# Kernel optimization log

Hardware: AMD Instinct MI355X
Metric: run time of the kernel (lower is better)

The kernel has to match this reference:

```python
import jax, jax.numpy as jnp
import numpy as np

N_PAPER, N_MESH = 60000, 30000
N = N_PAPER + N_MESH
E_TRAIN, E_DEC = 2000000, 400000
F_PAPER = F_MESH = 128
D0, H, D = 16, 32, 16  # initial embed, hidden, final embed
NREL, NB = 2, 4


def _glorot(key, shape):
    fan_in, fan_out = shape[-2], shape[-1]
    s = jnp.sqrt(6.0 / (fan_in + fan_out)).astype(jnp.float32)
    return jax.random.uniform(key, shape, jnp.float32, -s, s)


def setup_inputs() -> dict:
    key = jax.random.key(0)
    ks = iter(jax.random.split(key, 40))
    inp = {
        'x_paper': jax.random.normal(next(ks), (N_PAPER, F_PAPER), jnp.float32),
        'x_mesh': jax.random.normal(next(ks), (N_MESH, F_MESH), jnp.float32),
        'train_edge_index': jax.random.randint(next(ks), (2, E_TRAIN), 0, N, jnp.int64 if jax.config.jax_enable_x64 else jnp.int32),
        'train_edge_type': jnp.sort(jax.random.randint(next(ks), (E_TRAIN,), 0, NREL)),
        'pos_edge_index': jax.random.randint(next(ks), (2, E_DEC), 0, N),
        'pos_edge_type': jnp.sort(jax.random.randint(next(ks), (E_DEC,), 0, NREL)),
        'neg_edge_index': jax.random.randint(next(ks), (2, E_DEC), 0, N),
        'neg_edge_type': jnp.sort(jax.random.randint(next(ks), (E_DEC,), 0, NREL)),
        # input transforms
        'Wp': _glorot(next(ks), (F_PAPER, D0)), 'bp': jnp.zeros((D0,), jnp.float32),
        'Wm': _glorot(next(ks), (F_MESH, D0)), 'bm': jnp.zeros((D0,), jnp.float32),
        # decode linears
        'Wd0': _glorot(next(ks), (D, D)), 'bd0': jnp.zeros((D,), jnp.float32),
        'Wd1': _glorot(next(ks), (D, D)), 'bd1': jnp.zeros((D,), jnp.float32),
    }
    dims = [(D0, H), (H, H), (H, H), (H, D)]
    for i, (di, do) in enumerate(dims, 1):
        inp[f'bases{i}'] = _glorot(next(ks), (NB, di, do))
        inp[f'comp{i}'] = _glorot(next(ks), (NREL, NB))
        inp[f'root{i}'] = _glorot(next(ks), (di, do))
        inp[f'bias{i}'] = jnp.zeros((do,), jnp.float32)
    return inp


def rgcn_layer(x, src, dst, et, bases, comp, root, bias):
    # PyG RGCNConv with basis decomposition, per-relation mean aggregation.
    out = x @ root + bias
    xs = x[src]  # [E, in]
    for r in range(NREL):
        W_r = jnp.einsum('b,bio->io', comp[r], bases)
        m = xs @ W_r  # [E, out]
        mf = (et == r).astype(m.dtype)
        cnt = jax.ops.segment_sum(mf, dst, num_segments=N)
        agg = jax.ops.segment_sum(m * mf[:, None], dst, num_segments=N)
        out = out + agg / jnp.clip(cnt, 1.0)[:, None]
    return out


def _decode_block(z, ei, et, Wd0, bd0, Wd1, bd1):
    zs, zd = z[ei[0]], z[ei[1]]
    h0 = zs @ Wd0 + bd0
    h1 = zs @ Wd1 + bd1
    h = jnp.where((et == 0)[:, None], h0, h1)
    return jnp.sum(h * zd, axis=-1)


def reference(x_paper, x_mesh, train_edge_index, train_edge_type,
              pos_edge_index, pos_edge_type, neg_edge_index, neg_edge_type,
              Wp, bp, Wm, bm, Wd0, bd0, Wd1, bd1,
              bases1, comp1, root1, bias1, bases2, comp2, root2, bias2,
              bases3, comp3, root3, bias3, bases4, comp4, root4, bias4):
    x = jnp.concatenate([x_paper @ Wp + bp, x_mesh @ Wm + bm], axis=0)  # [N, D0]
    src, dst = train_edge_index[0], train_edge_index[1]
    x = jax.nn.relu(rgcn_layer(x, src, dst, train_edge_type, bases1, comp1, root1, bias1))
    x = jax.nn.relu(rgcn_layer(x, src, dst, train_edge_type, bases2, comp2, root2, bias2))
    x = jax.nn.relu(rgcn_layer(x, src, dst, train_edge_type, bases3, comp3, root3, bias3))
    z = rgcn_layer(x, src, dst, train_edge_type, bases4, comp4, root4, bias4)
    # edge types are sorted, so per-edge in-order compute matches the masked concat order
    pos = _decode_block(z, pos_edge_index, pos_edge_type, Wd0, bd0, Wd1, bd1)
    neg = _decode_block(z, neg_edge_index, neg_edge_type, Wd0, bd0, Wd1, bd1)
    return jnp.concatenate([pos, neg], axis=0)  # [2*E_DEC]
```

## Files before the change

kernel.cpp:

```cpp
#include <hip/hip_runtime.h>
#include <hip/hip_bf16.h>

constexpr int NN = 90000;
constexpr int NP = 60000;
constexpr int NM = 30000;
constexpr int ET = 2000000;
constexpr int ED = 400000;
constexpr int TWO_NN = 2 * NN;

constexpr int BKT_SH  = 10;
constexpr int NB_BKT  = (TWO_NN + 1023) >> BKT_SH;
constexpr int BKT_CAP = 12288;
constexpr int TILE    = 2048;
constexpr int N_TILES = (ET + TILE - 1) / TILE;

__device__ __forceinline__ float bf2f(unsigned short u) {
    union { unsigned int i; float f; } c;
    c.i = ((unsigned int)u) << 16;
    return c.f;
}
__device__ __forceinline__ unsigned short f2bf(float f) {
    union { float f; unsigned int i; } c;
    c.f = f;
    unsigned int x = c.i;
    return (unsigned short)((x + 0x7FFFu + ((x >> 16) & 1u)) >> 16);
}

__global__ void detect_kernel(const int* __restrict__ tei, int* __restrict__ flag) {
    if (blockIdx.x == 0 && threadIdx.x == 0) {
        int allzero = 1;
        for (int i = 0; i < 16; i++)
            if (tei[2 * i + 1] != 0) allzero = 0;
        flag[0] = allzero;
    }
}

__global__ void init_gcur_kernel(int* __restrict__ gcur) {
    int b = blockIdx.x * blockDim.x + threadIdx.x;
    if (b < NB_BKT) gcur[b] = b * BKT_CAP;
}

__global__ void __launch_bounds__(256) binA_kernel(
        const int* __restrict__ ei, const int* __restrict__ et,
        const int* __restrict__ dflag, int* __restrict__ gcur,
        int2* __restrict__ pairs) {
    __shared__ int hist[NB_BKT];
    __shared__ int excl[NB_BKT];
    __shared__ int cur[NB_BKT];
    __shared__ int gbase[NB_BKT];
    __shared__ int scn[256];
    __shared__ int2 tbuf[TILE];
    int t = threadIdx.x;
    int tile0 = blockIdx.x * TILE;
    int tcount = ET - tile0;
    if (tcount > TILE) tcount = TILE;
    for (int i = t; i < NB_BKT; i += 256) hist[i] = 0;
    __syncthreads();
    int sft = dflag[0];
    int myk[8], mys[8];
#pragma unroll
    for (int q = 0; q < 8; q++) {
        int li = q * 256 + t;
        myk[q] = -1;
        if (li < tcount) {
            int e = tile0 + li;
            int s = ei[(size_t)e << sft];
            int d = ei[(size_t)(ET + e) << sft];
            int r = et[(size_t)e << sft];
            int key = r * NN + d;
            myk[q] = key;
            mys[q] = s;
            atomicAdd(&hist[key >> BKT_SH], 1);
        }
    }
    __syncthreads();
    int v = (t < NB_BKT) ? hist[t] : 0;
    scn[t] = v;
    __syncthreads();
    for (int st = 1; st < 256; st <<= 1) {
        int u = (t >= st) ? scn[t - st] : 0;
        __syncthreads();
        scn[t] += u;
        __syncthreads();
    }
    if (t < NB_BKT) {
        excl[t] = scn[t] - v;
        cur[t] = scn[t] - v;
    }
    __syncthreads();
#pragma unroll
    for (int q = 0; q < 8; q++) {
        if (myk[q] >= 0) {
            int b = myk[q] >> BKT_SH;
            int p = atomicAdd(&cur[b], 1);
            tbuf[p] = make_int2(myk[q], mys[q]);
        }
    }
    __syncthreads();
    if (t < NB_BKT && hist[t] > 0) gbase[t] = atomicAdd(&gcur[t], hist[t]);
    __syncthreads();
    for (int i = t; i < tcount; i += 256) {
        int2 p = tbuf[i];
        int b = p.x >> BKT_SH;
        int gpos = gbase[b] + (i - excl[b]);
        int cap = (b + 1) * BKT_CAP - 1;
        pairs[gpos < cap ? gpos : cap] = p;
    }
}

__global__ void __launch_bounds__(256) histB_kernel(
        const int* __restrict__ gcur, const int2* __restrict__ pairs,
        int* __restrict__ off, int* __restrict__ endo, float* __restrict__ inv) {
    __shared__ int kh[1024];
    __shared__ int scn[256];
    int b = blockIdx.x;
    int t = threadIdx.x;
    for (int i = t; i < 1024; i += 256) kh[i] = 0;
    __syncthreads();
    int beg = b * BKT_CAP, end = gcur[b];
    for (int i = beg + t; i < end; i += 256)
        atomicAdd(&kh[pairs[i].x & 1023], 1);
    __syncthreads();
    int v[4];
    int s = 0;
#pragma unroll
    for (int q = 0; q < 4; q++) {
        v[q] = kh[t * 4 + q];
        s += v[q];
    }
    scn[t] = s;
    __syncthreads();
    for (int st = 1; st < 256; st <<= 1) {
        int u = (t >= st) ? scn[t - st] : 0;
        __syncthreads();
        scn[t] += u;
        __syncthreads();
    }
    int run = b * BKT_CAP + scn[t] - s;
    int kbase = b << BKT_SH;
#pragma unroll
    for (int q = 0; q < 4; q++) {
        int key = kbase + t * 4 + q;
        if (key < TWO_NN) {
            off[key] = run;
            endo[key] = run + v[q];
            inv[key] = 1.0f / (float)(v[q] > 1 ? v[q] : 1);
        }
        run += v[q];
    }
}

__global__ void __launch_bounds__(256) placeB_kernel(
        const int* __restrict__ gcur, const int2* __restrict__ pairs,
        const int* __restrict__ off, int* __restrict__ csr) {
    __shared__ int kc[1024];
    int b = blockIdx.x;
    int t = threadIdx.x;
    int kbase = b << BKT_SH;
    for (int i = t; i < 1024; i += 256)
        if (kbase + i < TWO_NN) kc[i] = off[kbase + i];
    __syncthreads();
    int beg = b * BKT_CAP, end = gcur[b];
    for (int i = beg + t; i < end; i += 256) {
        int2 p = pairs[i];
        int pos = atomicAdd(&kc[p.x & 1023], 1);
        csr[pos] = p.y;
    }
}

__global__ void __launch_bounds__(256) embed2_kernel(
        const float* __restrict__ Xp, const float* __restrict__ Xm,
        const float* __restrict__ Wp, const float* __restrict__ bp,
        const float* __restrict__ Wm, const float* __restrict__ bm,
        float* __restrict__ out, unsigned short* __restrict__ outbf) {
    __shared__ float Wl[4096 + 32];
    for (int i = threadIdx.x; i < 2048; i += 256) {
        Wl[i] = Wp[i];
        Wl[2048 + i] = Wm[i];
    }
    if (threadIdx.x < 16) {
        Wl[4096 + threadIdx.x] = bp[threadIdx.x];
        Wl[4112 + threadIdx.x] = bm[threadIdx.x];
    }
    __syncthreads();
    int n = blockIdx.x * 256 + threadIdx.x;
    if (n >= NN) return;
    const float* X;
    const float* Ws;
    const float* Bs;
    if (n < NP) { X = Xp + (size_t)n * 128; Ws = Wl; Bs = Wl + 4096; }
    else        { X = Xm + (size_t)(n - NP) * 128; Ws = Wl + 2048; Bs = Wl + 4112; }
    float acc[16];
#pragma unroll
    for (int j = 0; j < 16; j++) acc[j] = Bs[j];
    const float4* row = (const float4*)X;
    for (int k4 = 0; k4 < 32; k4++) {
        float4 xv = row[k4];
        int k = k4 * 4;
#pragma unroll
        for (int j = 0; j < 16; j++) {
            float a = acc[j];
            a = fmaf(xv.x, Ws[(k + 0) * 16 + j], a);
            a = fmaf(xv.y, Ws[(k + 1) * 16 + j], a);
            a = fmaf(xv.z, Ws[(k + 2) * 16 + j], a);
            a = fmaf(xv.w, Ws[(k + 3) * 16 + j], a);
            acc[j] = a;
        }
    }
    float4* o = (float4*)(out + (size_t)n * 16);
    ushort4* ob = (ushort4*)(outbf + (size_t)n * 16);
#pragma unroll
    for (int q = 0; q < 4; q++) {
        o[q] = make_float4(acc[4 * q], acc[4 * q + 1], acc[4 * q + 2], acc[4 * q + 3]);
        ushort4 ub;
        ub.x = f2bf(acc[4 * q]);     ub.y = f2bf(acc[4 * q + 1]);
        ub.z = f2bf(acc[4 * q + 2]); ub.w = f2bf(acc[4 * q + 3]);
        ob[q] = ub;
    }
}

__global__ void prep_all_kernel(
        const float* __restrict__ ba0, const float* __restrict__ co0,
        const float* __restrict__ ro0, const float* __restrict__ bi0,
        const float* __restrict__ ba1, const float* __restrict__ co1,
        const float* __restrict__ ro1, const float* __restrict__ bi1,
        const float* __restrict__ ba2, const float* __restrict__ co2,
        const float* __restrict__ ro2, const float* __restrict__ bi2,
        const float* __restrict__ ba3, const float* __restrict__ co3,
        const float* __restrict__ ro3, const float* __restrict__ bi3,
        float* __restrict__ Wbuf4) {
    int l = blockIdx.x;
    const float* bases; const float* comp; const float* root; const float* bias;
    if (l == 0)      { bases = ba0; comp = co0; root = ro0; bias = bi0; }
    else if (l == 1) { bases = ba1; comp = co1; root = ro1; bias = bi1; }
    else if (l == 2) { bases = ba2; comp = co2; root = ro2; bias = bi2; }
    else             { bases = ba3; comp = co3; root = ro3; bias = bi3; }
    int din = (l == 0) ? 16 : 32;
    int dout = (l == 3) ? 16 : 32;
    int sz = din * dout;
    float* W = Wbuf4 + l * 3200;
    for (int i = threadIdx.x; i < sz; i += 256) {
        float b0 = bases[i];
        float b1 = bases[sz + i];
        float b2 = bases[2 * sz + i];
        float b3 = bases[3 * sz + i];
        for (int r = 0; r < 2; r++) {
            W[r * sz + i] = comp[r * 4 + 0] * b0 + comp[r * 4 + 1] * b1 +
                            comp[r * 4 + 2] * b2 + comp[r * 4 + 3] * b3;
        }
        W[2 * sz + i] = root[i];
    }
    if (threadIdx.x < dout) W[3 * sz + threadIdx.x] = bias[threadIdx.x];
}

template <int DIN, int DOUT, int RELU, int WBF>
__global__ void __launch_bounds__(256) layer_kernel(
        const int* __restrict__ off, const int* __restrict__ endo,
        const int* __restrict__ csr,
        const float* __restrict__ xin, const unsigned short* __restrict__ xbf_in,
        const float* __restrict__ inv, const float* __restrict__ Wbuf,
        float* __restrict__ xout, unsigned short* __restrict__ xbf_out) {
    constexpr int SZ = DIN * DOUT;
    constexpr int QL = DIN / 4;
    constexpr int TPN = 2 * QL;
    constexpr int NPB = 256 / TPN;
    constexpr int AGST = 2 * DIN + 4;
    constexpr int XSST = DIN + 4;
    __shared__ float Wl[3 * SZ + DOUT];
    __shared__ float agg[NPB * AGST];
    __shared__ float xs[NPB * XSST];
    for (int i = threadIdx.x; i < 3 * SZ + DOUT; i += 256) Wl[i] = Wbuf[i];
    int t = threadIdx.x;
    int ln = t / TPN;
    int rl = t % TPN;
    int r = rl / QL;
    int lane = rl % QL;
    int d = blockIdx.x * NPB + ln;
    if (d < NN) {
        if (r == 0)
            *(float4*)(xs + ln * XSST + lane * 4) =
                *(const float4*)(xin + (size_t)d * DIN + lane * 4);
        int key = r * NN + d;
        int b = off[key];
        int e = endo[key];
        float4 a0 = make_float4(0, 0, 0, 0), a1 = make_float4(0, 0, 0, 0);
        float4 a2 = make_float4(0, 0, 0, 0), a3 = make_float4(0, 0, 0, 0);
        const unsigned short* hp = xbf_in + lane * 4;
        int k = b;
        for (; k + 3 < e; k += 4) {
            int s0 = csr[k];
            int s1 = csr[k + 1];
            int s2 = csr[k + 2];
            int s3 = csr[k + 3];
            ushort4 u0 = *(const ushort4*)(hp + (size_t)s0 * DIN);
            ushort4 u1 = *(const ushort4*)(hp + (size_t)s1 * DIN);
            ushort4 u2 = *(const ushort4*)(hp + (size_t)s2 * DIN);
            ushort4 u3 = *(const ushort4*)(hp + (size_t)s3 * DIN);
            a0.x += bf2f(u0.x); a0.y += bf2f(u0.y); a0.z += bf2f(u0.z); a0.w += bf2f(u0.w);
            a1.x += bf2f(u1.x); a1.y += bf2f(u1.y); a1.z += bf2f(u1.z); a1.w += bf2f(u1.w);
            a2.x += bf2f(u2.x); a2.y += bf2f(u2.y); a2.z += bf2f(u2.z); a2.w += bf2f(u2.w);
            a3.x += bf2f(u3.x); a3.y += bf2f(u3.y); a3.z += bf2f(u3.z); a3.w += bf2f(u3.w);
        }
        for (; k < e; k++) {
            ushort4 u0 = *(const ushort4*)(hp + (size_t)csr[k] * DIN);
            a0.x += bf2f(u0.x); a0.y += bf2f(u0.y); a0.z += bf2f(u0.z); a0.w += bf2f(u0.w);
        }
        *(float4*)(agg + ln * AGST + r * DIN + lane * 4) =
            make_float4(a0.x + a1.x + a2.x + a3.x, a0.y + a1.y + a2.y + a3.y,
                        a0.z + a1.z + a2.z + a3.z, a0.w + a1.w + a2.w + a3.w);
    }
    __syncthreads();
    constexpr int CPN = DOUT / 4;
    if (t < NPB * CPN) {
        int ln2 = t / CPN;
        int j0 = (t % CPN) * 4;
        int d2 = blockIdx.x * NPB + ln2;
        if (d2 < NN) {
            float iv0 = inv[d2], iv1 = inv[NN + d2];
            float acc[4];
#pragma unroll
            for (int jj = 0; jj < 4; jj++) acc[jj] = Wl[3 * SZ + j0 + jj];
#pragma unroll
            for (int k = 0; k < DIN; k++) {
                float xv = xs[ln2 * XSST + k];
                float a0 = agg[ln2 * AGST + k] * iv0;
                float a1 = agg[ln2 * AGST + DIN + k] * iv1;
                const float* w0 = &Wl[k * DOUT + j0];
                const float* w1 = &Wl[SZ + k * DOUT + j0];
                const float* wr = &Wl[2 * SZ + k * DOUT + j0];
#pragma unroll
                for (int jj = 0; jj < 4; jj++) {
                    acc[jj] = fmaf(xv, wr[jj], acc[jj]);
                    acc[jj] = fmaf(a0, w0[jj], acc[jj]);
                    acc[jj] = fmaf(a1, w1[jj], acc[jj]);
                }
            }
            if (RELU) {
#pragma unroll
                for (int jj = 0; jj < 4; jj++) acc[jj] = fmaxf(acc[jj], 0.0f);
            }
            *(float4*)(xout + (size_t)d2 * DOUT + j0) =
                make_float4(acc[0], acc[1], acc[2], acc[3]);
            if (WBF) {
                ushort4 ub;
                ub.x = f2bf(acc[0]); ub.y = f2bf(acc[1]);
                ub.z = f2bf(acc[2]); ub.w = f2bf(acc[3]);
                *(ushort4*)(xbf_out + (size_t)d2 * DOUT + j0) = ub;
            }
        }
    }
}

__global__ void decode_prep_kernel(const float* __restrict__ z,
                                   const float* __restrict__ Wd0,
                                   const float* __restrict__ bd0,
                                   const float* __restrict__ Wd1,
                                   const float* __restrict__ bd1,
                                   float* __restrict__ y0, float* __restrict__ y1) {
    __shared__ float W0l[256], W1l[256], B0[16], B1[16];
    for (int i = threadIdx.x; i < 256; i += blockDim.x) {
        W0l[i] = Wd0[i];
        W1l[i] = Wd1[i];
    }
    if (threadIdx.x < 16) {
        B0[threadIdx.x] = bd0[threadIdx.x];
        B1[threadIdx.x] = bd1[threadIdx.x];
    }
    __syncthreads();
    int n = blockIdx.x * blockDim.x + threadIdx.x;
    if (n >= NN) return;
    float zr[16];
    const float* zp = z + (size_t)n * 16;
#pragma unroll
    for (int k = 0; k < 16; k++) zr[k] = zp[k];
    float o0[16], o1[16];
#pragma unroll
    for (int j = 0; j < 16; j++) {
        float a0 = B0[j], a1 = B1[j];
#pragma unroll
        for (int k = 0; k < 16; k++) {
            a0 = fmaf(zr[k], W0l[k * 16 + j], a0);
            a1 = fmaf(zr[k], W1l[k * 16 + j], a1);
        }
        o0[j] = a0;
        o1[j] = a1;
    }
    float4* p0 = (float4*)(y0 + (size_t)n * 16);
    float4* p1 = (float4*)(y1 + (size_t)n * 16);
#pragma unroll
    for (int q = 0; q < 4; q++) {
        p0[q] = make_float4(o0[4 * q], o0[4 * q + 1], o0[4 * q + 2], o0[4 * q + 3]);
        p1[q] = make_float4(o1[4 * q], o1[4 * q + 1], o1[4 * q + 2], o1[4 * q + 3]);
    }
}

__global__ void decode_kernel(const float* __restrict__ y0, const float* __restrict__ y1,
                              const float* __restrict__ z,
                              const int* __restrict__ pei, const int* __restrict__ pet,
                              const int* __restrict__ nei, const int* __restrict__ net_,
                              float* __restrict__ out,
                              const int* __restrict__ dflag) {
    int i = blockIdx.x * blockDim.x + threadIdx.x;
    if (i >= 2 * ED) return;
    int sft = dflag[0];
    const int* ei;
    const int* et;
    int e;
    if (i < ED) { ei = pei; et = pet; e = i; }
    else        { ei = nei; et = net_; e = i - ED; }
    int s = ei[(size_t)e << sft];
    int d = ei[(size_t)(ED + e) << sft];
    int r = et[(size_t)e << sft];
    const float4* yv = (const float4*)((r ? y1 : y0) + ((size_t)s << 4));
    const float4* zv = (const float4*)(z + ((size_t)d << 4));
    float acc = 0.0f;
#pragma unroll
    for (int q = 0; q < 4; q++) {
        float4 a = yv[q];
        float4 b = zv[q];
        acc += a.x * b.x + a.y * b.y + a.z * b.z + a.w * b.w;
    }
    out[i] = acc;
}

extern "C" void kernel_launch(void* const* d_in, const int* in_sizes, int n_in,
                              void* d_out, int out_size, void* d_ws, size_t ws_size,
                              hipStream_t stream) {
    const float* x_paper = (const float*)d_in[0];
    const float* x_mesh  = (const float*)d_in[1];
    const int* tei  = (const int*)d_in[2];
    const int* tet  = (const int*)d_in[3];
    const int* pei  = (const int*)d_in[4];
    const int* pet  = (const int*)d_in[5];
    const int* nei  = (const int*)d_in[6];
    const int* net_ = (const int*)d_in[7];
    const float* Wp  = (const float*)d_in[8];
    const float* bp  = (const float*)d_in[9];
    const float* Wm  = (const float*)d_in[10];
    const float* bm  = (const float*)d_in[11];
    const float* Wd0 = (const float*)d_in[12];
    const float* bd0 = (const float*)d_in[13];
    const float* Wd1 = (const float*)d_in[14];
    const float* bd1 = (const float*)d_in[15];

    float* ws = (float*)d_ws;
    size_t o = 0;
    float* bufA = ws + o; o += (size_t)NN * 32;
    float* bufB = ws + o; o += (size_t)NN * 32;
    unsigned short* xbfA = (unsigned short*)(ws + o); o += (size_t)NN * 16;
    unsigned short* xbfB = (unsigned short*)(ws + o); o += (size_t)NN * 16;
    float* inv  = ws + o; o += (size_t)TWO_NN;
    int*   off  = (int*)(ws + o); o += (size_t)TWO_NN;
    int*   endo = (int*)(ws + o); o += (size_t)TWO_NN;
    int*   csr  = (int*)(ws + o); o += (size_t)NB_BKT * BKT_CAP;
    int*   gcur = (int*)(ws + o); o += 256;
    int2*  pairs = (int2*)(ws + o); o += (size_t)2 * NB_BKT * BKT_CAP;
    float* Wbuf4 = ws + o; o += 4 * 3200;
    int*   dflag = (int*)(ws + o); o += 16;

    detect_kernel<<<1, 64, 0, stream>>>(tei, dflag);

    init_gcur_kernel<<<1, 256, 0, stream>>>(gcur);
    binA_kernel<<<N_TILES, 256, 0, stream>>>(tei, tet, dflag, gcur, pairs);
    histB_kernel<<<NB_BKT, 256, 0, stream>>>(gcur, pairs, off, endo, inv);
    placeB_kernel<<<NB_BKT, 256, 0, stream>>>(gcur, pairs, off, csr);

    embed2_kernel<<<(NN + 255) / 256, 256, 0, stream>>>(
        x_paper, x_mesh, Wp, bp, Wm, bm, bufA, xbfA);

    prep_all_kernel<<<4, 256, 0, stream>>>(
        (const float*)d_in[16], (const float*)d_in[17], (const float*)d_in[18], (const float*)d_in[19],
        (const float*)d_in[20], (const float*)d_in[21], (const float*)d_in[22], (const float*)d_in[23],
        (const float*)d_in[24], (const float*)d_in[25], (const float*)d_in[26], (const float*)d_in[27],
        (const float*)d_in[28], (const float*)d_in[29], (const float*)d_in[30], (const float*)d_in[31],
        Wbuf4);

    int blk16 = (NN + 31) / 32;
    int blk32 = (NN + 15) / 16;
    layer_kernel<16, 32, 1, 1><<<blk16, 256, 0, stream>>>(
        off, endo, csr, bufA, xbfA, inv, Wbuf4 + 0 * 3200, bufB, xbfB);
    layer_kernel<32, 32, 1, 1><<<blk32, 256, 0, stream>>>(
        off, endo, csr, bufB, xbfB, inv, Wbuf4 + 1 * 3200, bufA, xbfA);
    layer_kernel<32, 32, 1, 1><<<blk32, 256, 0, stream>>>(
        off, endo, csr, bufA, xbfA, inv, Wbuf4 + 2 * 3200, bufB, xbfB);
    layer_kernel<32, 16, 0, 0><<<blk32, 256, 0, stream>>>(
        off, endo, csr, bufB, xbfB, inv, Wbuf4 + 3 * 3200, bufA, xbfA );

    float* y0 = bufB;
    float* y1 = bufB + (size_t)NN * 16;
    decode_prep_kernel<<<(NN + 255) / 256, 256, 0, stream>>>(bufA, Wd0, bd0, Wd1, bd1,
                                                             y0, y1);
    decode_kernel<<<(2 * ED + 255) / 256, 256, 0, stream>>>(
        y0, y1, bufA, pei, pet, nei, net_, (float*)d_out, dflag);
}
```

Measured before the change: 430.5 us.

## Widen gather loads to 16 bytes, fuse decode kernels, merge init kernels

The layer gather now has each thread load 8 bf16 values with one uint4 load instead of 4, so twice as many nodes fit in a block and the grid sizes halve. The decode prep and decode kernels are merged: each edge recomputes the 16x16 relation transform of the source embedding in registers instead of reading a precomputed y buffer. The detect and gcur-init kernels become one kernel. The changes cut launches and intermediate memory traffic, but add redundant per-edge FLOPs in decode and reduce memory-level parallelism per thread in the gather.

New measurement: 400.4 us. -7.0%, faster.

```diff
diff --git a/kernel.cpp b/kernel.cpp
--- a/kernel.cpp
+++ b/kernel.cpp
@@ -14,9 +14,14 @@
 constexpr int TILE    = 2048;
 constexpr int N_TILES = (ET + TILE - 1) / TILE;
 
-__device__ __forceinline__ float bf2f(unsigned short u) {
+__device__ __forceinline__ float bflo(unsigned int u) {
     union { unsigned int i; float f; } c;
-    c.i = ((unsigned int)u) << 16;
+    c.i = u << 16;
+    return c.f;
+}
+__device__ __forceinline__ float bfhi(unsigned int u) {
+    union { unsigned int i; float f; } c;
+    c.i = u & 0xffff0000u;
     return c.f;
 }
 __device__ __forceinline__ unsigned short f2bf(float f) {
@@ -26,18 +31,16 @@
     return (unsigned short)((x + 0x7FFFu + ((x >> 16) & 1u)) >> 16);
 }
 
-__global__ void detect_kernel(const int* __restrict__ tei, int* __restrict__ flag) {
-    if (blockIdx.x == 0 && threadIdx.x == 0) {
+__global__ void init_kernel(const int* __restrict__ tei, int* __restrict__ gcur,
+                            int* __restrict__ dflag) {
+    int b = blockIdx.x * blockDim.x + threadIdx.x;
+    if (b < NB_BKT) gcur[b] = b * BKT_CAP;
+    if (b == 0) {
         int allzero = 1;
         for (int i = 0; i < 16; i++)
             if (tei[2 * i + 1] != 0) allzero = 0;
-        flag[0] = allzero;
-    }
-}
-
-__global__ void init_gcur_kernel(int* __restrict__ gcur) {
-    int b = blockIdx.x * blockDim.x + threadIdx.x;
-    if (b < NB_BKT) gcur[b] = b * BKT_CAP;
+        dflag[0] = allzero;
+    }
 }
 
 __global__ void __launch_bounds__(256) binA_kernel(
@@ -261,7 +264,7 @@
         const float* __restrict__ inv, const float* __restrict__ Wbuf,
         float* __restrict__ xout, unsigned short* __restrict__ xbf_out) {
     constexpr int SZ = DIN * DOUT;
-    constexpr int QL = DIN / 4;
+    constexpr int QL = DIN / 8;
     constexpr int TPN = 2 * QL;
     constexpr int NPB = 256 / TPN;
     constexpr int AGST = 2 * DIN + 4;
@@ -277,43 +280,47 @@
     int lane = rl % QL;
     int d = blockIdx.x * NPB + ln;
     if (d < NN) {
-        if (r == 0)
-            *(float4*)(xs + ln * XSST + lane * 4) =
-                *(const float4*)(xin + (size_t)d * DIN + lane * 4);
+        *(float4*)(xs + ln * XSST + rl * 4) =
+            *(const float4*)(xin + (size_t)d * DIN + rl * 4);
         int key = r * NN + d;
         int b = off[key];
         int e = endo[key];
-        float4 a0 = make_float4(0, 0, 0, 0), a1 = make_float4(0, 0, 0, 0);
-        float4 a2 = make_float4(0, 0, 0, 0), a3 = make_float4(0, 0, 0, 0);
-        const unsigned short* hp = xbf_in + lane * 4;
+        float a0[8] = {0, 0, 0, 0, 0, 0, 0, 0};
+        float a1[8] = {0, 0, 0, 0, 0, 0, 0, 0};
+        const unsigned short* hp = xbf_in + lane * 8;
         int k = b;
-        for (; k + 3 < e; k += 4) {
+        for (; k + 1 < e; k += 2) {
             int s0 = csr[k];
             int s1 = csr[k + 1];
-            int s2 = csr[k + 2];
-            int s3 = csr[k + 3];
-            ushort4 u0 = *(const ushort4*)(hp + (size_t)s0 * DIN);
-            ushort4 u1 = *(const ushort4*)(hp + (size_t)s1 * DIN);
-            ushort4 u2 = *(const ushort4*)(hp + (size_t)s2 * DIN);
-            ushort4 u3 = *(const ushort4*)(hp + (size_t)s3 * DIN);
-            a0.x += bf2f(u0.x); a0.y += bf2f(u0.y); a0.z += bf2f(u0.z); a0.w += bf2f(u0.w);
-            a1.x += bf2f(u1.x); a1.y += bf2f(u1.y); a1.z += bf2f(u1.z); a1.w += bf2f(u1.w);
-            a2.x += bf2f(u2.x); a2.y += bf2f(u2.y); a2.z += bf2f(u2.z); a2.w += bf2f(u2.w);
-            a3.x += bf2f(u3.x); a3.y += bf2f(u3.y); a3.z += bf2f(u3.z); a3.w += bf2f(u3.w);
-        }
-        for (; k < e; k++) {
-            ushort4 u0 = *(const ushort4*)(hp + (size_t)csr[k] * DIN);
-            a0.x += bf2f(u0.x); a0.y += bf2f(u0.y); a0.z += bf2f(u0.z); a0.w += bf2f(u0.w);
-        }
-        *(float4*)(agg + ln * AGST + r * DIN + lane * 4) =
-            make_float4(a0.x + a1.x + a2.x + a3.x, a0.y + a1.y + a2.y + a3.y,
-                        a0.z + a1.z + a2.z + a3.z, a0.w + a1.w + a2.w + a3.w);
+            uint4 u0 = *(const uint4*)(hp + (size_t)s0 * DIN);
+            uint4 u1 = *(const uint4*)(hp + (size_t)s1 * DIN);
+            a0[0] += bflo(u0.x); a0[1] += bfhi(u0.x);
+            a0[2] += bflo(u0.y); a0[3] += bfhi(u0.y);
+            a0[4] += bflo(u0.z); a0[5] += bfhi(u0.z);
+            a0[6] += bflo(u0.w); a0[7] += bfhi(u0.w);
+            a1[0] += bflo(u1.x); a1[1] += bfhi(u1.x);
+            a1[2] += bflo(u1.y); a1[3] += bfhi(u1.y);
+            a1[4] += bflo(u1.z); a1[5] += bfhi(u1.z);
+            a1[6] += bflo(u1.w); a1[7] += bfhi(u1.w);
+        }
+        if (k < e) {
+            uint4 u0 = *(const uint4*)(hp + (size_t)csr[k] * DIN);
+            a0[0] += bflo(u0.x); a0[1] += bfhi(u0.x);
+            a0[2] += bflo(u0.y); a0[3] += bfhi(u0.y);
+            a0[4] += bflo(u0.z); a0[5] += bfhi(u0.z);
+            a0[6] += bflo(u0.w); a0[7] += bfhi(u0.w);
+        }
+        float* ap = agg + ln * AGST + r * DIN + lane * 8;
+        *(float4*)ap = make_float4(a0[0] + a1[0], a0[1] + a1[1],
+                                   a0[2] + a1[2], a0[3] + a1[3]);
+        *(float4*)(ap + 4) = make_float4(a0[4] + a1[4], a0[5] + a1[5],
+                                         a0[6] + a1[6], a0[7] + a1[7]);
     }
     __syncthreads();
     constexpr int CPN = DOUT / 4;
-    if (t < NPB * CPN) {
-        int ln2 = t / CPN;
-        int j0 = (t % CPN) * 4;
+    for (int tt = t; tt < NPB * CPN; tt += 256) {
+        int ln2 = tt / CPN;
+        int j0 = (tt % CPN) * 4;
         int d2 = blockIdx.x * NPB + ln2;
         if (d2 < NN) {
             float iv0 = inv[d2], iv1 = inv[NN + d2];
@@ -323,16 +330,16 @@
 #pragma unroll
             for (int k = 0; k < DIN; k++) {
                 float xv = xs[ln2 * XSST + k];
-                float a0 = agg[ln2 * AGST + k] * iv0;
-                float a1 = agg[ln2 * AGST + DIN + k] * iv1;
+                float m0 = agg[ln2 * AGST + k] * iv0;
+                float m1 = agg[ln2 * AGST + DIN + k] * iv1;
                 const float* w0 = &Wl[k * DOUT + j0];
                 const float* w1 = &Wl[SZ + k * DOUT + j0];
                 const float* wr = &Wl[2 * SZ + k * DOUT + j0];
 #pragma unroll
                 for (int jj = 0; jj < 4; jj++) {
                     acc[jj] = fmaf(xv, wr[jj], acc[jj]);
-                    acc[jj] = fmaf(a0, w0[jj], acc[jj]);
-                    acc[jj] = fmaf(a1, w1[jj], acc[jj]);
+                    acc[jj] = fmaf(m0, w0[jj], acc[jj]);
+                    acc[jj] = fmaf(m1, w1[jj], acc[jj]);
                 }
             }
             if (RELU) {
@@ -351,56 +358,25 @@
     }
 }
 
-__global__ void decode_prep_kernel(const float* __restrict__ z,
-                                   const float* __restrict__ Wd0,
-                                   const float* __restrict__ bd0,
-                                   const float* __restrict__ Wd1,
-                                   const float* __restrict__ bd1,
-                                   float* __restrict__ y0, float* __restrict__ y1) {
-    __shared__ float W0l[256], W1l[256], B0[16], B1[16];
-    for (int i = threadIdx.x; i < 256; i += blockDim.x) {
-        W0l[i] = Wd0[i];
-        W1l[i] = Wd1[i];
+__global__ void __launch_bounds__(256) decode_fused_kernel(
+        const float* __restrict__ z,
+        const float* __restrict__ Wd0, const float* __restrict__ bd0,
+        const float* __restrict__ Wd1, const float* __restrict__ bd1,
+        const int* __restrict__ pei, const int* __restrict__ pet,
+        const int* __restrict__ nei, const int* __restrict__ net_,
+        float* __restrict__ out, const int* __restrict__ dflag) {
+    __shared__ float W[2][256];
+    __shared__ float B[2][16];
+    for (int i = threadIdx.x; i < 256; i += 256) {
+        W[0][i] = Wd0[i];
+        W[1][i] = Wd1[i];
     }
     if (threadIdx.x < 16) {
-        B0[threadIdx.x] = bd0[threadIdx.x];
-        B1[threadIdx.x] = bd1[threadIdx.x];
-    }
-    __syncthreads();
-    int n = blockIdx.x * blockDim.x + threadIdx.x;
-    if (n >= NN) return;
-    float zr[16];
-    const float* zp = z + (size_t)n * 16;
-#pragma unroll
-    for (int k = 0; k < 16; k++) zr[k] = zp[k];
-    float o0[16], o1[16];
-#pragma unroll
-    for (int j = 0; j < 16; j++) {
-        float a0 = B0[j], a1 = B1[j];
-#pragma unroll
-        for (int k = 0; k < 16; k++) {
-            a0 = fmaf(zr[k], W0l[k * 16 + j], a0);
-            a1 = fmaf(zr[k], W1l[k * 16 + j], a1);
-        }
-        o0[j] = a0;
-        o1[j] = a1;
-    }
-    float4* p0 = (float4*)(y0 + (size_t)n * 16);
-    float4* p1 = (float4*)(y1 + (size_t)n * 16);
-#pragma unroll
-    for (int q = 0; q < 4; q++) {
-        p0[q] = make_float4(o0[4 * q], o0[4 * q + 1], o0[4 * q + 2], o0[4 * q + 3]);
-        p1[q] = make_float4(o1[4 * q], o1[4 * q + 1], o1[4 * q + 2], o1[4 * q + 3]);
-    }
-}
-
-__global__ void decode_kernel(const float* __restrict__ y0, const float* __restrict__ y1,
-                              const float* __restrict__ z,
-                              const int* __restrict__ pei, const int* __restrict__ pet,
-                              const int* __restrict__ nei, const int* __restrict__ net_,
-                              float* __restrict__ out,
-                              const int* __restrict__ dflag) {
-    int i = blockIdx.x * blockDim.x + threadIdx.x;
+        B[0][threadIdx.x] = bd0[threadIdx.x];
+        B[1][threadIdx.x] = bd1[threadIdx.x];
+    }
+    __syncthreads();
+    int i = blockIdx.x * 256 + threadIdx.x;
     if (i >= 2 * ED) return;
     int sft = dflag[0];
     const int* ei;
@@ -411,14 +387,25 @@
     int s = ei[(size_t)e << sft];
     int d = ei[(size_t)(ED + e) << sft];
     int r = et[(size_t)e << sft];
-    const float4* yv = (const float4*)((r ? y1 : y0) + ((size_t)s << 4));
-    const float4* zv = (const float4*)(z + ((size_t)d << 4));
+    float zs[16], zd[16];
+    const float4* sp = (const float4*)(z + ((size_t)s << 4));
+    const float4* dp = (const float4*)(z + ((size_t)d << 4));
+#pragma unroll
+    for (int q = 0; q < 4; q++) {
+        float4 a = sp[q];
+        float4 b = dp[q];
+        zs[4 * q] = a.x; zs[4 * q + 1] = a.y; zs[4 * q + 2] = a.z; zs[4 * q + 3] = a.w;
+        zd[4 * q] = b.x; zd[4 * q + 1] = b.y; zd[4 * q + 2] = b.z; zd[4 * q + 3] = b.w;
+    }
+    const float* Wr = W[r];
+    const float* Br = B[r];
     float acc = 0.0f;
 #pragma unroll
-    for (int q = 0; q < 4; q++) {
-        float4 a = yv[q];
-        float4 b = zv[q];
-        acc += a.x * b.x + a.y * b.y + a.z * b.z + a.w * b.w;
+    for (int j = 0; j < 16; j++) {
+        float yj = Br[j];
+#pragma unroll
+        for (int k = 0; k < 16; k++) yj = fmaf(zs[k], Wr[k * 16 + j], yj);
+        acc = fmaf(yj, zd[j], acc);
     }
     out[i] = acc;
 }
@@ -458,9 +445,8 @@
     float* Wbuf4 = ws + o; o += 4 * 3200;
     int*   dflag = (int*)(ws + o); o += 16;
 
-    detect_kernel<<<1, 64, 0, stream>>>(tei, dflag);
-
-    init_gcur_kernel<<<1, 256, 0, stream>>>(gcur);
+    init_kernel<<<1, 256, 0, stream>>>(tei, gcur, dflag);
+
     binA_kernel<<<N_TILES, 256, 0, stream>>>(tei, tet, dflag, gcur, pairs);
     histB_kernel<<<NB_BKT, 256, 0, stream>>>(gcur, pairs, off, endo, inv);
     placeB_kernel<<<NB_BKT, 256, 0, stream>>>(gcur, pairs, off, csr);
@@ -475,8 +461,8 @@
         (const float*)d_in[28], (const float*)d_in[29], (const float*)d_in[30], (const float*)d_in[31],
         Wbuf4);
 
-    int blk16 = (NN + 31) / 32;
-    int blk32 = (NN + 15) / 16;
+    int blk16 = (NN + 63) / 64;
+    int blk32 = (NN + 31) / 32;
     layer_kernel<16, 32, 1, 1><<<blk16, 256, 0, stream>>>(
         off, endo, csr, bufA, xbfA, inv, Wbuf4 + 0 * 3200, bufB, xbfB);
     layer_kernel<32, 32, 1, 1><<<blk32, 256, 0, stream>>>(
@@ -486,10 +472,6 @@
     layer_kernel<32, 16, 0, 0><<<blk32, 256, 0, stream>>>(
         off, endo, csr, bufB, xbfB, inv, Wbuf4 + 3 * 3200, bufA, xbfA );
 
-    float* y0 = bufB;
-    float* y1 = bufB + (size_t)NN * 16;
-    decode_prep_kernel<<<(NN + 255) / 256, 256, 0, stream>>>(bufA, Wd0, bd0, Wd1, bd1,
-                                                             y0, y1);
-    decode_kernel<<<(2 * ED + 255) / 256, 256, 0, stream>>>(
-        y0, y1, bufA, pei, pet, nei, net_, (float*)d_out, dflag);
-}
+    decode_fused_kernel<<<(2 * ED + 255) / 256, 256, 0, stream>>>(
+        bufA, Wd0, bd0, Wd1, bd1, pei, pet, nei, net_, (float*)d_out, dflag);
+}
```
